# Performance work log

Hardware: AMD Instinct MI355X
Metric: run time of the kernel (lower is better)

Reference implementation:

```python
import jax, jax.numpy as jnp
import numpy as np

HEADS = 12
DIM_HEAD = 64
INNER = HEADS * DIM_HEAD  # 768
DIM = 512
KS = 3


def setup_inputs() -> dict:
    key = jax.random.key(0)
    ks = jax.random.split(key, 5)
    B, H, W = 8, 32, 32
    N = H * W + 1  # +1 cls token -> has_cls path
    x = jax.random.normal(ks[0], (B, N, DIM), dtype=jnp.float32)
    w_qkv = jax.random.normal(ks[1], (3 * INNER, DIM), dtype=jnp.float32) * (DIM ** -0.5)
    w_dw = jax.random.normal(ks[2], (DIM, 1, KS, KS), dtype=jnp.float32) * (1.0 / KS)
    w_out = jax.random.normal(ks[3], (DIM, INNER), dtype=jnp.float32) * (INNER ** -0.5)
    b_out = jax.random.normal(ks[4], (DIM,), dtype=jnp.float32) * 0.01
    return {"x": x, "w_qkv": w_qkv, "w_dw": w_dw, "w_out": w_out,
            "b_out": b_out, "h_feat": H, "w_feat": W}


def reference(x, w_qkv, w_dw, w_out, b_out, h_feat, w_feat):
    B, N, C = x.shape
    scale = DIM_HEAD ** -0.5
    # qkv projection (Linear, no bias): torch weight layout (out,in)
    qkv = jnp.einsum('bnc,oc->bno', x, w_qkv)  # (B,N,3*INNER)
    q, k, v = jnp.split(qkv, 3, axis=-1)

    def split_heads(t):
        return t.reshape(B, N, HEADS, DIM_HEAD).transpose(0, 2, 1, 3)  # (B,H,N,d)

    q, k, v = map(split_heads, (q, k, v))
    dots = jnp.einsum('bhid,bhjd->bhij', q, k) * scale
    attn = jax.nn.softmax(dots, axis=-1)
    out_attn = jnp.einsum('bhij,bhjd->bhid', attn, v)
    out_attn = out_attn.transpose(0, 2, 1, 3).reshape(B, N, INNER)

    has_cls = (N == h_feat * w_feat + 1)  # static
    spatial = x[:, 1:, :] if has_cls else x
    spatial_2d = spatial.transpose(0, 2, 1).reshape(B, C, h_feat, w_feat)
    # depthwise conv, padding = ks//2 (SAME for odd ks, stride 1)
    loc = jax.lax.conv_general_dilated(
        spatial_2d, w_dw, window_strides=(1, 1), padding='SAME',
        feature_group_count=C,
        dimension_numbers=('NCHW', 'OIHW', 'NCHW'))
    local_out = loc.reshape(B, C, h_feat * w_feat).transpose(0, 2, 1)  # (B,hw,C)
    if has_cls:
        cls_out = x[:, :1, :INNER]  # C < INNER so this is the full cls token
        local_out = jnp.concatenate([cls_out, local_out], axis=1)  # (B,N,C)
    if local_out.shape[-1] < INNER:
        out = out_attn + jnp.pad(
            local_out, ((0, 0), (0, 0), (0, INNER - local_out.shape[-1])))
    else:
        out = out_attn
    # output Linear (dropout=0 in eval)
    return jnp.einsum('bni,oi->bno', out, w_out) + b_out
```

## Files before the change

kernel.cpp:

```cpp
#include <hip/hip_runtime.h>
#include <hip/hip_bf16.h>
#include <stdint.h>
#include <math.h>

typedef __bf16 bf16;
typedef __bf16 bf16x8 __attribute__((ext_vector_type(8)));
typedef float f32x4 __attribute__((ext_vector_type(4)));
typedef short s4 __attribute__((ext_vector_type(4)));

#define QSCALE 0.1803368801111f


__device__ __forceinline__ void gload_lds16(const void* g, void* l) {
  typedef const __attribute__((address_space(1))) char g_char;
  typedef __attribute__((address_space(3))) char l_char;
  g_char* gp = (g_char*)(uintptr_t)g;
  l_char* lp = (l_char*)(uint32_t)(uintptr_t)l;
  __builtin_amdgcn_global_load_lds(gp, lp, 16, 0, 0);
}

__device__ __forceinline__ float fexp2(float x) {
#if __has_builtin(__builtin_amdgcn_exp2f)
  return __builtin_amdgcn_exp2f(x);
#else
  return exp2f(x);
#endif
}

__device__ __forceinline__ float frcp(float x) {
#if __has_builtin(__builtin_amdgcn_rcpf)
  return __builtin_amdgcn_rcpf(x);
#else
  return 1.f / x;
#endif
}

__device__ __forceinline__ uint32_t pk2(float a, float b) {
  union { bf16 h; unsigned short u; } ua, ub;
  ua.h = (bf16)a; ub.h = (bf16)b;
  return (uint32_t)ua.u | ((uint32_t)ub.u << 16);
}

__device__ __forceinline__ float ubf(uint32_t u) {
  union { uint32_t i; float f; } v;
  v.i = u << 16;
  return v.f;
}

__device__ __forceinline__ f32x4 pv_mfma(s4 a, s4 b, f32x4 c) {
#if __has_builtin(__builtin_amdgcn_mfma_f32_16x16x16bf16_1k)
  return __builtin_amdgcn_mfma_f32_16x16x16bf16_1k(a, b, c, 0, 0, 0);
#else
  asm volatile("v_mfma_f32_16x16x16_bf16 %0, %1, %2, %0" : "+v"(c) : "v"(a), "v"(b));
  return c;
#endif
}

__global__ __launch_bounds__(256) void k_prep(const float* __restrict__ x,
                                              const float* __restrict__ wqkv,
                                              const float* __restrict__ wout,
                                              bf16* __restrict__ xb, bf16* __restrict__ wqkvb,
                                              bf16* __restrict__ woutb, bf16* __restrict__ vP) {
  int i = blockIdx.x * 256 + threadIdx.x;
  const float* src = nullptr;
  bf16* dst = nullptr;
  int q = i;
  bool zero = false;
  if (i < 1064960) {
    if (i < 1049600) src = x; else zero = true;
    dst = xb;
  } else if (i < 1064960 + 294912) {
    q = i - 1064960; src = wqkv; dst = wqkvb;
  } else if (i < 1064960 + 294912 + 98304) {
    q = i - (1064960 + 294912); src = wout; dst = woutb;
  } else {
    int qq = i - (1064960 + 294912 + 98304);
    int z = qq * 4;
    int head = z >> 12;
    int off = z & 4095;
    uint2 zz; zz.x = 0u; zz.y = 0u;
    *(uint2*)&vP[(size_t)head * 69632 + 65536 + off] = zz;
    return;
  }
  float4 v = make_float4(0.f, 0.f, 0.f, 0.f);
  if (!zero) v = *(const float4*)&src[(size_t)q * 4];
  uint2 p;
  p.x = pk2(v.x, v.y);
  p.y = pk2(v.z, v.w);
  *(uint2*)&dst[(size_t)q * 4] = p;
}

template <int EPI, int BN>
__global__ __launch_bounds__(256) void k_gemm(const bf16* __restrict__ A,
                                              const bf16* __restrict__ Bt, int K,
                                              bf16* __restrict__ q, bf16* __restrict__ kk,
                                              bf16* __restrict__ vt,
                                              const float* __restrict__ bias,
                                              float* __restrict__ out) {
  __shared__ __attribute__((aligned(16))) bf16 sA[128 * 64];
  __shared__ __attribute__((aligned(16))) bf16 sB[BN * 64];
  constexpr int MF = (BN == 128) ? 4 : 2;
  constexpr int WROWS = (BN == 128) ? 64 : 32;
  const int tid = threadIdx.x;
  const int lane = tid & 63;
  const int w = tid >> 6;
  const int wr = (BN == 128) ? (w >> 1) : w;
  const int wc = (BN == 128) ? (w & 1) : 0;
  const int tn = blockIdx.x, tm = blockIdx.y;
  const int l15 = lane & 15, l4 = lane >> 4;
  const int srow = lane >> 3, sslot = lane & 7;

  f32x4 acc[MF][4] = {};

  const int Ksteps = K >> 6;
  for (int kt = 0; kt < Ksteps; ++kt) {
    __syncthreads();
#pragma unroll
    for (int i = 0; i < 4; ++i) {
      int row = w * 32 + i * 8 + srow;
      int clog = sslot ^ (row & 7);
      gload_lds16(A + ((size_t)(tm * 128 + row) * K + kt * 64 + clog * 8),
                  &sA[(w * 32 + i * 8) * 64]);
    }
#pragma unroll
    for (int i = 0; i < BN / 32; ++i) {
      int row = w * (BN / 4) + i * 8 + srow;
      int clog = sslot ^ (row & 7);
      gload_lds16(Bt + ((size_t)(tn * BN + row) * K + kt * 64 + clog * 8),
                  &sB[(w * (BN / 4) + i * 8) * 64]);
    }
    __syncthreads();
#pragma unroll
    for (int ks = 0; ks < 2; ++ks) {
      bf16x8 af[MF], bfr[4];
#pragma unroll
      for (int mf = 0; mf < MF; ++mf) {
        int row = wr * WROWS + mf * 16 + l15;
        int phys = (ks * 4 + l4) ^ (row & 7);
        af[mf] = *(const bf16x8*)&sA[row * 64 + phys * 8];
      }
#pragma unroll
      for (int nf = 0; nf < 4; ++nf) {
        int row = wc * 64 + nf * 16 + l15;
        int phys = (ks * 4 + l4) ^ (row & 7);
        bfr[nf] = *(const bf16x8*)&sB[row * 64 + phys * 8];
      }
#pragma unroll
      for (int mf = 0; mf < MF; ++mf)
#pragma unroll
        for (int nf = 0; nf < 4; ++nf)
          acc[mf][nf] =
              __builtin_amdgcn_mfma_f32_16x16x32_bf16(bfr[nf], af[mf], acc[mf][nf], 0, 0, 0);
    }
  }

  const int RbaseL = tm * 128 + wr * WROWS + l15;
  const int CbaseL = tn * BN + wc * 64 + l4 * 4;
#pragma unroll
  for (int mf = 0; mf < MF; ++mf) {
    int R = RbaseL + mf * 16;
    if (R >= 8200) continue;
    if (EPI == 0) {
      int b = R / 1025;
      int n = R - b * 1025;
      int kvq = n >> 2, e = n & 3;
#pragma unroll
      for (int nf = 0; nf < 4; ++nf) {
        int Cc0 = CbaseL + nf * 16;
        int seg = (Cc0 >= 1536) ? 2 : (Cc0 >= 768 ? 1 : 0);
        int inner = Cc0 - seg * 768;
        int h = inner >> 6, d0 = inner & 63;
        if (seg == 2) {
          bf16* vb = &vt[(((size_t)(b * 12 + h) * 272 + kvq) * 64 + d0) * 4 + e];
#pragma unroll
          for (int r = 0; r < 4; ++r) vb[r * 4] = (bf16)acc[mf][nf][r];
        } else {
          bf16* dst = seg ? kk : q;
          float scl = seg ? 1.f : QSCALE;
          uint2 p;
          p.x = pk2(acc[mf][nf][0] * scl, acc[mf][nf][1] * scl);
          p.y = pk2(acc[mf][nf][2] * scl, acc[mf][nf][3] * scl);
          *(uint2*)&dst[(((size_t)b * 12 + h) * 1088 + n) * 64 + d0] = p;
        }
      }
    } else {
#pragma unroll
      for (int nf = 0; nf < 4; ++nf) {
        int Cc0 = CbaseL + nf * 16;
        float4 bz = *(const float4*)&bias[Cc0];
        float4 o4;
        o4.x = acc[mf][nf][0] + bz.x;
        o4.y = acc[mf][nf][1] + bz.y;
        o4.z = acc[mf][nf][2] + bz.z;
        o4.w = acc[mf][nf][3] + bz.w;
        *(float4*)&out[(size_t)R * 512 + Cc0] = o4;
      }
    }
  }
}

__global__ __launch_bounds__(256) void k_flash(const bf16* __restrict__ qg,
                                               const bf16* __restrict__ kg,
                                               const bf16* __restrict__ vpg,
                                               bf16* __restrict__ outb) {
  __shared__ __attribute__((aligned(16))) bf16 sK[2][64 * 64];
  __shared__ __attribute__((aligned(16))) bf16 sVP[2][16 * 256];
  const int tid = threadIdx.x, lane = tid & 63, w = tid >> 6;
  const int l15 = lane & 15, l4 = lane >> 4;
  const int wg = blockIdx.x;
  const int logical = (wg & 7) * 204 + (wg >> 3);
  const int bh = logical / 17, qgp = logical - bh * 17;
  const int b = bh / 12, h = bh - b * 12;
  const int srow = lane >> 3, sslot = lane & 7;

  size_t qoff = ((size_t)bh * 1088 + qgp * 64 + w * 16 + l15) * 64 + l4 * 8;
  const bf16x8 qf0 = *(const bf16x8*)&qg[qoff];
  const bf16x8 qf1 = *(const bf16x8*)&qg[qoff + 32];

  float lreg = 0.f;
  f32x4 oa[4] = {};

  const int px0 = (l4 ^ (l15 & 7)) * 8;
  const int px1 = ((4 + l4) ^ (l15 & 7)) * 8;

  const int rowA = w * 16 + srow, rowB = rowA + 8;
  const int clogA = sslot ^ (rowA & 7), clogB = sslot ^ (rowB & 7);
  const bf16* kS1 = kg + ((size_t)bh * 1088 + rowA) * 64 + clogA * 8;
  const bf16* kS2 = kg + ((size_t)bh * 1088 + rowB) * 64 + clogB * 8;
  const bf16* vS1 = vpg + (size_t)bh * 69632 + w * 1024 + lane * 8;
  const bf16* vS2 = vS1 + 512;
  const int kD1 = rowA * 64, kD2 = rowB * 64;
  const int vD1 = w * 1024 + lane * 8, vD2 = vD1 + 512;

  auto STAGE = [&](int bi, int t) {
    size_t o = (size_t)t * 4096;
    gload_lds16(kS1 + o, &sK[bi][kD1]);
    gload_lds16(kS2 + o, &sK[bi][kD2]);
    gload_lds16(vS1 + o, &sVP[bi][vD1]);
    gload_lds16(vS2 + o, &sVP[bi][vD2]);
  };

  STAGE(0, 0);
  int cur = 0;

  for (int t = 0; t < 17; ++t) {
    asm volatile("s_waitcnt vmcnt(0)" ::: "memory");
    __builtin_amdgcn_s_barrier();
    __builtin_amdgcn_sched_barrier(0);
    if (t < 16) STAGE(cur ^ 1, t + 1);

    const bf16* kb_ = sK[cur];
    const bf16* vpb = sVP[cur];

    f32x4 sc[4] = {};
    __builtin_amdgcn_s_setprio(1);
#pragma unroll
    for (int jt = 0; jt < 4; ++jt) {
      bf16x8 a0 = *(const bf16x8*)&kb_[(jt * 16 + l15) * 64 + px0];
      sc[jt] = __builtin_amdgcn_mfma_f32_16x16x32_bf16(a0, qf0, sc[jt], 0, 0, 0);
    }
#pragma unroll
    for (int jt = 0; jt < 4; ++jt) {
      bf16x8 a1 = *(const bf16x8*)&kb_[(jt * 16 + l15) * 64 + px1];
      sc[jt] = __builtin_amdgcn_mfma_f32_16x16x32_bf16(a1, qf1, sc[jt], 0, 0, 0);
    }
    __builtin_amdgcn_s_setprio(0);

    if (t == 16) {
#pragma unroll
      for (int jt = 0; jt < 4; ++jt)
#pragma unroll
        for (int r = 0; r < 4; ++r) {
          if (jt == 0 && r == 0)
            sc[jt][r] = (l4 == 0) ? sc[jt][r] : -INFINITY;
          else
            sc[jt][r] = -INFINITY;
        }
    }

    union { uint32_t u[2]; s4 v; } pa[4];
    float lsum = 0.f;
#pragma unroll
    for (int jt = 0; jt < 4; ++jt) {
      float p0 = fexp2(sc[jt][0] - 8.0f);
      float p1 = fexp2(sc[jt][1] - 8.0f);
      float p2 = fexp2(sc[jt][2] - 8.0f);
      float p3 = fexp2(sc[jt][3] - 8.0f);
      lsum += (p0 + p1) + (p2 + p3);
      pa[jt].u[0] = pk2(p0, p1);
      pa[jt].u[1] = pk2(p2, p3);
    }
    lreg += lsum;

    __builtin_amdgcn_s_setprio(1);
#pragma unroll
    for (int jt = 0; jt < 4; ++jt)
#pragma unroll
      for (int db = 0; db < 4; ++db) {
        s4 vf = *(const s4*)&vpb[((jt * 4 + l4) * 64 + db * 16 + l15) * 4];
        oa[db] = pv_mfma(pa[jt].v, vf, oa[db]);
      }
    __builtin_amdgcn_s_setprio(0);
    cur ^= 1;
  }

  float ls = lreg;
  ls += __shfl_xor(ls, 16);
  ls += __shfl_xor(ls, 32);
  float linv = frcp(ls);
#pragma unroll
  for (int r = 0; r < 4; ++r) {
    float ir = __shfl(linv, l4 * 4 + r);
    int n = qgp * 64 + w * 16 + l4 * 4 + r;
    if (n >= 1025) continue;
#pragma unroll
    for (int db = 0; db < 4; ++db)
      outb[((size_t)b * 1025 + n) * 768 + h * 64 + db * 16 + l15] = (bf16)(oa[db][r] * ir);
  }
}

__global__ __launch_bounds__(256) void k_local(const float* __restrict__ x,
                                               const float* __restrict__ wdw,
                                               bf16* __restrict__ outb) {
  const int b = blockIdx.x, y = blockIdx.y, xseg = blockIdx.z;
  const int c = threadIdx.x * 2;
  const int x0 = xseg * 8;
  const bool hm = (y > 0), hp = (y < 31);
  float wa[9], wb[9];
#pragma unroll
  for (int k = 0; k < 9; ++k) {
    wa[k] = wdw[(size_t)c * 9 + k];
    wb[k] = wdw[(size_t)(c + 1) * 9 + k];
  }
  const float* xb = x + ((size_t)b * 1025 + 1) * 512 + c;
  float A0 = 0.f, B0 = 0.f, A1 = 0.f, B1 = 0.f;
  for (int cc = x0 - 1; cc <= x0 + 8; ++cc) {
    float2 v0 = make_float2(0.f, 0.f), v1 = v0, v2 = v0;
    if (cc >= 0 && cc < 32) {
      v1 = *(const float2*)&xb[((size_t)y * 32 + cc) * 512];
      if (hm) v0 = *(const float2*)&xb[((size_t)(y - 1) * 32 + cc) * 512];
      if (hp) v2 = *(const float2*)&xb[((size_t)(y + 1) * 32 + cc) * 512];
    }
    float t0a = v0.x * wa[0] + v1.x * wa[3] + v2.x * wa[6];
    float t1a = v0.x * wa[1] + v1.x * wa[4] + v2.x * wa[7];
    float t2a = v0.x * wa[2] + v1.x * wa[5] + v2.x * wa[8];
    float t0b = v0.y * wb[0] + v1.y * wb[3] + v2.y * wb[6];
    float t1b = v0.y * wb[1] + v1.y * wb[4] + v2.y * wb[7];
    float t2b = v0.y * wb[2] + v1.y * wb[5] + v2.y * wb[8];
    int oc = cc - 1;
    if (oc >= x0 && oc <= x0 + 7) {
      size_t o = ((size_t)b * 1025 + 1 + y * 32 + oc) * 768 + c;
      uint32_t old = *(const uint32_t*)&outb[o];
      *(uint32_t*)&outb[o] =
          pk2(ubf(old & 0xffffu) + (A0 + t2a), ubf(old >> 16) + (A1 + t2b));
    }
    A0 = B0 + t1a; B0 = t0a;
    A1 = B1 + t1b; B1 = t0b;
  }
  if (y == 0 && xseg == 0) {
    size_t o = ((size_t)b * 1025) * 768 + c;
    float2 xc = *(const float2*)&x[((size_t)b * 1025) * 512 + c];
    uint32_t old = *(const uint32_t*)&outb[o];
    *(uint32_t*)&outb[o] = pk2(ubf(old & 0xffffu) + xc.x, ubf(old >> 16) + xc.y);
  }
}

extern "C" void kernel_launch(void* const* d_in, const int* in_sizes, int n_in,
                              void* d_out, int out_size, void* d_ws, size_t ws_size,
                              hipStream_t stream) {
  const float* x = (const float*)d_in[0];
  const float* w_qkv = (const float*)d_in[1];
  const float* w_dw = (const float*)d_in[2];
  const float* w_out = (const float*)d_in[3];
  const float* b_out = (const float*)d_in[4];
  float* out = (float*)d_out;

  char* ws = (char*)d_ws;
  size_t off = 0;
  auto alloc = [&](size_t bytes) {
    char* p = ws + off;
    off = (off + bytes + 255) & ~(size_t)255;
    return p;
  };
  bf16* xb    = (bf16*)alloc((size_t)8320 * 512 * 2);
  bf16* wqkvb = (bf16*)alloc((size_t)2304 * 512 * 2);
  bf16* woutb = (bf16*)alloc((size_t)512 * 768 * 2);
  bf16* qb    = (bf16*)alloc((size_t)96 * 1088 * 64 * 2);
  bf16* kb    = (bf16*)alloc((size_t)96 * 1088 * 64 * 2);
  bf16* vP    = (bf16*)alloc((size_t)96 * 272 * 64 * 4 * 2);
  bf16* outb  = (bf16*)alloc((size_t)8320 * 768 * 2);

  k_prep<<<6080, 256, 0, stream>>>(x, w_qkv, w_out, xb, wqkvb, woutb, vP);
  k_gemm<0, 128><<<dim3(18, 65), 256, 0, stream>>>(xb, wqkvb, 512, qb, kb, vP, nullptr, nullptr);
  k_flash<<<1632, 256, 0, stream>>>(qb, kb, vP, outb);
  k_local<<<dim3(8, 32, 4), 256, 0, stream>>>(x, w_dw, outb);
  k_gemm<1, 64><<<dim3(8, 65), 256, 0, stream>>>(outb, woutb, 768, nullptr, nullptr, nullptr,
                                                 b_out, out);
}
```

Before: 146.8 us.

## Double-buffer GEMM LDS tiles with K-step 32 to overlap loads and MFMA

Restructures the k_gemm main loop to use two LDS buffers of half the K depth (32 instead of 64). The next tile's global-to-LDS loads are issued before the current tile's MFMAs, so memory latency overlaps compute, and one barrier per step replaces two. It also raises wave priority around the MFMA block and changes the swizzle to a 4-chunk XOR. The cost is twice as many loop iterations, each with less work per barrier, and a full vmcnt(0) wait that may still expose latency.

```diff
diff --git a/kernel.cpp b/kernel.cpp
--- a/kernel.cpp
+++ b/kernel.cpp
@@ -97,8 +97,8 @@
                                               bf16* __restrict__ vt,
                                               const float* __restrict__ bias,
                                               float* __restrict__ out) {
-  __shared__ __attribute__((aligned(16))) bf16 sA[128 * 64];
-  __shared__ __attribute__((aligned(16))) bf16 sB[BN * 64];
+  __shared__ __attribute__((aligned(16))) bf16 sA[2][128 * 32];
+  __shared__ __attribute__((aligned(16))) bf16 sB[2][BN * 32];
   constexpr int MF = (BN == 128) ? 4 : 2;
   constexpr int WROWS = (BN == 128) ? 64 : 32;
   const int tid = threadIdx.x;
@@ -108,50 +108,60 @@
   const int wc = (BN == 128) ? (w & 1) : 0;
   const int tn = blockIdx.x, tm = blockIdx.y;
   const int l15 = lane & 15, l4 = lane >> 4;
-  const int srow = lane >> 3, sslot = lane & 7;
 
   f32x4 acc[MF][4] = {};
 
-  const int Ksteps = K >> 6;
+  const int srow = lane >> 2, schunk = lane & 3;
+  const int rA = w * 32 + srow;
+  const bf16* aS = A + ((size_t)(tm * 128 + rA)) * K + ((schunk ^ (rA & 3)) * 8);
+  const int rB = (BN == 128) ? (w * 32 + srow) : (w * 16 + srow);
+  const bf16* bS = Bt + ((size_t)(tn * BN + rB)) * K + ((schunk ^ (rB & 3)) * 8);
+
+  auto STAGE = [&](int bi, int kt) {
+    size_t o = (size_t)kt * 32;
+    gload_lds16(aS + o, &sA[bi][(w * 32) * 32]);
+    gload_lds16(aS + (size_t)16 * K + o, &sA[bi][(w * 32 + 16) * 32]);
+    if constexpr (BN == 128) {
+      gload_lds16(bS + o, &sB[bi][(w * 32) * 32]);
+      gload_lds16(bS + (size_t)16 * K + o, &sB[bi][(w * 32 + 16) * 32]);
+    } else {
+      gload_lds16(bS + o, &sB[bi][(w * 16) * 32]);
+    }
+  };
+
+  STAGE(0, 0);
+  int cur = 0;
+  const int Ksteps = K >> 5;
   for (int kt = 0; kt < Ksteps; ++kt) {
-    __syncthreads();
-#pragma unroll
-    for (int i = 0; i < 4; ++i) {
-      int row = w * 32 + i * 8 + srow;
-      int clog = sslot ^ (row & 7);
-      gload_lds16(A + ((size_t)(tm * 128 + row) * K + kt * 64 + clog * 8),
-                  &sA[(w * 32 + i * 8) * 64]);
-    }
-#pragma unroll
-    for (int i = 0; i < BN / 32; ++i) {
-      int row = w * (BN / 4) + i * 8 + srow;
-      int clog = sslot ^ (row & 7);
-      gload_lds16(Bt + ((size_t)(tn * BN + row) * K + kt * 64 + clog * 8),
-                  &sB[(w * (BN / 4) + i * 8) * 64]);
-    }
-    __syncthreads();
-#pragma unroll
-    for (int ks = 0; ks < 2; ++ks) {
-      bf16x8 af[MF], bfr[4];
-#pragma unroll
-      for (int mf = 0; mf < MF; ++mf) {
-        int row = wr * WROWS + mf * 16 + l15;
-        int phys = (ks * 4 + l4) ^ (row & 7);
-        af[mf] = *(const bf16x8*)&sA[row * 64 + phys * 8];
-      }
-#pragma unroll
-      for (int nf = 0; nf < 4; ++nf) {
-        int row = wc * 64 + nf * 16 + l15;
-        int phys = (ks * 4 + l4) ^ (row & 7);
-        bfr[nf] = *(const bf16x8*)&sB[row * 64 + phys * 8];
-      }
-#pragma unroll
-      for (int mf = 0; mf < MF; ++mf)
-#pragma unroll
-        for (int nf = 0; nf < 4; ++nf)
-          acc[mf][nf] =
-              __builtin_amdgcn_mfma_f32_16x16x32_bf16(bfr[nf], af[mf], acc[mf][nf], 0, 0, 0);
-    }
+    asm volatile("s_waitcnt vmcnt(0)" ::: "memory");
+    __builtin_amdgcn_s_barrier();
+    __builtin_amdgcn_sched_barrier(0);
+    if (kt + 1 < Ksteps) STAGE(cur ^ 1, kt + 1);
+
+    const bf16* a_ = sA[cur];
+    const bf16* b_ = sB[cur];
+    bf16x8 af[MF], bfr[4];
+#pragma unroll
+    for (int mf = 0; mf < MF; ++mf) {
+      int row = wr * WROWS + mf * 16 + l15;
+      int phys = l4 ^ (row & 3);
+      af[mf] = *(const bf16x8*)&a_[row * 32 + phys * 8];
+    }
+#pragma unroll
+    for (int nf = 0; nf < 4; ++nf) {
+      int row = wc * 64 + nf * 16 + l15;
+      int phys = l4 ^ (row & 3);
+      bfr[nf] = *(const bf16x8*)&b_[row * 32 + phys * 8];
+    }
+    __builtin_amdgcn_s_setprio(1);
+#pragma unroll
+    for (int mf = 0; mf < MF; ++mf)
+#pragma unroll
+      for (int nf = 0; nf < 4; ++nf)
+        acc[mf][nf] =
+            __builtin_amdgcn_mfma_f32_16x16x32_bf16(bfr[nf], af[mf], acc[mf][nf], 0, 0, 0);
+    __builtin_amdgcn_s_setprio(0);
+    cur ^= 1;
   }
 
   const int RbaseL = tm * 128 + wr * WROWS + l15;
```

Result: no change. 146.4 us (-0.3%).
